# Performance work log

Hardware: AMD Instinct MI355X
Metric: run time of the kernel (lower is better)

Reference implementation:

```python
import jax, jax.numpy as jnp
import numpy as np

NUM_EXPERTS = 8
TOP_K = 2


def setup_inputs() -> dict:
    key = jax.random.key(0)
    k1, k2, k3, k4, k5 = jax.random.split(key, 5)
    H, F, E = 1024, 4096, NUM_EXPERTS
    s = 0.02
    return {
        "hidden_states": jax.random.normal(k1, (2, 2048, H), jnp.float32),
        "w_router": jax.random.normal(k2, (E, H), jnp.float32) * s,
        "w1": jax.random.normal(k3, (E, F, H), jnp.float32) * s,
        "w2": jax.random.normal(k4, (E, H, F), jnp.float32) * s,
        "w3": jax.random.normal(k5, (E, F, H), jnp.float32) * s,
    }


def reference(hidden_states, w_router, w1, w2, w3):
    B, S, H = hidden_states.shape
    x = hidden_states.reshape(-1, H)  # [T, H]
    T = x.shape[0]
    # router (nn.Linear, no bias): logits = x @ W^T
    router_logits = x @ w_router.T  # [T, E]
    probs = jax.nn.softmax(router_logits.astype(jnp.float32), axis=-1)
    top_w, top_e = jax.lax.top_k(probs, TOP_K)  # [T, K]
    top_w = top_w / jnp.sum(top_w, axis=-1, keepdims=True)
    top_w = top_w.astype(x.dtype)
    # dense per-token gate matrix [T, E]; zero where expert not selected
    gates = jnp.zeros((T, NUM_EXPERTS), x.dtype).at[
        jnp.arange(T)[:, None], top_e
    ].add(top_w)
    out = jnp.zeros_like(x)
    for e in range(NUM_EXPERTS):  # fixed small expert loop
        h = jax.nn.silu(x @ w1[e].T) * (x @ w3[e].T)  # [T, F]
        out = out + gates[:, e:e + 1] * (h @ w2[e].T)
    return out.reshape(B, S, H), router_logits
```

## Files before the change

kernel.cpp:

```cpp
#include <hip/hip_runtime.h>
#include <hip/hip_bf16.h>
#include <stdint.h>

#define T_TOK 4096
#define H_DIM 1024
#define F_DIM 4096
#define NE 8
#define MG_BLKS 40

typedef float    f32x4  __attribute__((ext_vector_type(4)));
typedef __bf16   bf16x8 __attribute__((ext_vector_type(8)));
typedef uint16_t u16x8  __attribute__((ext_vector_type(8)));

#define AS1 __attribute__((address_space(1)))
#define AS3 __attribute__((address_space(3)))

__device__ __forceinline__ uint16_t f2bf(float f) {
  return __builtin_bit_cast(uint16_t, __float2bfloat16(f));
}

__device__ __forceinline__ void gld16(const void* g, void* l) {
  __builtin_amdgcn_global_load_lds((const AS1 void*)g, (AS3 void*)l, 16, 0, 0);
}

__device__ __forceinline__ bf16x8 ldsB_frag(const float* tile, int row, int kg) {
  const int p0 = (2 * kg) ^ (row & 15);
  const int p1 = (2 * kg + 1) ^ (row & 15);
  const f32x4 v0 = *(const f32x4*)&tile[row * 64 + p0 * 4];
  const f32x4 v1 = *(const f32x4*)&tile[row * 64 + p1 * 4];
  u16x8 ub;
#pragma unroll
  for (int j = 0; j < 4; ++j) { ub[j] = f2bf(v0[j]); ub[j + 4] = f2bf(v1[j]); }
  return __builtin_bit_cast(bf16x8, ub);
}

__global__ __launch_bounds__(256) void router_k(
    const float* __restrict__ x, const float* __restrict__ wr,
    float* __restrict__ logits, uint16_t* __restrict__ xb,
    int* __restrict__ pairTok, float* __restrict__ pairGate,
    int* __restrict__ tokSlot, int* __restrict__ cnt)
{
  const int lane = threadIdx.x & 63;
  const int wid  = threadIdx.x >> 6;
  const int t    = blockIdx.x * 4 + wid;

  const float* xp = x + (size_t)t * H_DIM + lane * 16;
  f32x4 xv[4];
#pragma unroll
  for (int i = 0; i < 4; ++i) xv[i] = *(const f32x4*)(xp + 4 * i);

  u16x8 o0, o1;
#pragma unroll
  for (int j = 0; j < 4; ++j) {
    o0[j] = f2bf(xv[0][j]); o0[j + 4] = f2bf(xv[1][j]);
    o1[j] = f2bf(xv[2][j]); o1[j + 4] = f2bf(xv[3][j]);
  }
  uint16_t* xbp = xb + (size_t)t * H_DIM + lane * 16;
  *(u16x8*)xbp       = o0;
  *(u16x8*)(xbp + 8) = o1;

  float s[NE];
#pragma unroll
  for (int e = 0; e < NE; ++e) {
    const float* wp = wr + e * H_DIM + lane * 16;
    float acc = 0.f;
#pragma unroll
    for (int i = 0; i < 4; ++i) {
      f32x4 wv = *(const f32x4*)(wp + 4 * i);
#pragma unroll
      for (int j = 0; j < 4; ++j) acc += xv[i][j] * wv[j];
    }
#pragma unroll
    for (int off = 32; off > 0; off >>= 1) acc += __shfl_xor(acc, off, 64);
    s[e] = acc;
  }

  if (lane == 0) {
#pragma unroll
    for (int e = 0; e < NE; ++e) logits[t * NE + e] = s[e];
    int e1 = 0;
#pragma unroll
    for (int e = 1; e < NE; ++e) if (s[e] > s[e1]) e1 = e;
    int e2 = (e1 == 0) ? 1 : 0;
#pragma unroll
    for (int e = 0; e < NE; ++e)
      if (e != e1 && e != e2 && s[e] > s[e2]) e2 = e;
    const float d  = s[e2] - s[e1];
    const float g1 = 1.f / (1.f + __expf(d));
    const float g2 = 1.f - g1;
    int i1 = atomicAdd(cnt + e1, 1);
    pairTok[e1 * T_TOK + i1] = t;  pairGate[e1 * T_TOK + i1] = g1;
    int i2 = atomicAdd(cnt + e2, 1);
    pairTok[e2 * T_TOK + i2] = t;  pairGate[e2 * T_TOK + i2] = g2;
    int4 sl; sl.x = e1; sl.y = i1; sl.z = e2; sl.w = i2;
    ((int4*)tokSlot)[t] = sl;
  }
}

__global__ void prefix_k(const int* __restrict__ cnt, int* __restrict__ base) {
  if (threadIdx.x == 0) {
    int b = 0;
#pragma unroll
    for (int e = 0; e < NE; ++e) { base[e] = b; b += (cnt[e] + 255) & ~255; }
    base[NE] = b;
  }
}

__global__ __launch_bounds__(256, 2) void ffn1_k(
    const uint16_t* __restrict__ xb, const float* __restrict__ w1,
    const float* __restrict__ w3, uint16_t* __restrict__ hbuf,
    const int* __restrict__ pairTok, const float* __restrict__ pairGate,
    const int* __restrict__ cnt, const int* __restrict__ base)
{
  const int mg0 = blockIdx.y * 256;
  if (mg0 >= base[NE]) return;
  int e = 0;
#pragma unroll
  for (int k = 1; k < NE; ++k) if (mg0 >= base[k]) e = k;
  const int m0   = mg0 - base[e];
  const int cnte = cnt[e];
  const int n0   = blockIdx.x * 64;
  const int tid  = threadIdx.x;
  const int lane = tid & 63;
  const int wid  = tid >> 6;
  const int wm   = (wid >> 1) * 128;
  const int wn   = (wid & 1) * 32;

  __shared__ __align__(16) uint16_t lsA [256 * 64];
  __shared__ __align__(16) float    lsB1[ 64 * 64];
  __shared__ __align__(16) float    lsB3[ 64 * 64];

  const float* w1e = w1 + (size_t)e * F_DIM * H_DIM;
  const float* w3e = w3 + (size_t)e * F_DIM * H_DIM;

  const uint16_t* asrc[8];
#pragma unroll
  for (int q = 0; q < 8; ++q) {
    const int c = q * 256 + tid;
    const int row = c >> 3, pos = c & 7;
    const int kc  = pos ^ (row & 7);
    int ar = m0 + row; if (ar >= cnte) ar = cnte - 1;
    const int tok = pairTok[e * T_TOK + ar];
    asrc[q] = xb + (size_t)tok * H_DIM + kc * 8;
  }
  const float* b1src[4];
  const float* b3src[4];
#pragma unroll
  for (int q = 0; q < 4; ++q) {
    const int c = q * 256 + tid;
    const int row = c >> 4, pos = c & 15;
    const int kc  = pos ^ (row & 15);
    b1src[q] = w1e + (size_t)(n0 + row) * H_DIM + kc * 4;
    b3src[q] = w3e + (size_t)(n0 + row) * H_DIM + kc * 4;
  }

  const f32x4 fz = {0.f, 0.f, 0.f, 0.f};
  f32x4 acc1[8][2], acc3[8][2];
#pragma unroll
  for (int i = 0; i < 8; ++i)
#pragma unroll
    for (int j = 0; j < 2; ++j) { acc1[i][j] = fz; acc3[i][j] = fz; }

  for (int kt = 0; kt < H_DIM; kt += 64) {
    __syncthreads();
#pragma unroll
    for (int q = 0; q < 8; ++q)
      gld16(asrc[q] + kt, &lsA[(q * 256 + tid) * 8]);
#pragma unroll
    for (int q = 0; q < 4; ++q) {
      gld16(b1src[q] + kt, &lsB1[(q * 256 + tid) * 4]);
      gld16(b3src[q] + kt, &lsB3[(q * 256 + tid) * 4]);
    }
    __syncthreads();
#pragma unroll
    for (int ks = 0; ks < 2; ++ks) {
      const int kg = ks * 4 + (lane >> 4);
      bf16x8 af[8], b1f[2], b3f[2];
#pragma unroll
      for (int i = 0; i < 8; ++i) {
        const int ar = wm + i * 16 + (lane & 15);
        af[i] = *(const bf16x8*)&lsA[ar * 64 + ((kg ^ (ar & 7)) * 8)];
      }
#pragma unroll
      for (int j = 0; j < 2; ++j) {
        const int br = wn + j * 16 + (lane & 15);
        b1f[j] = ldsB_frag(lsB1, br, kg);
        b3f[j] = ldsB_frag(lsB3, br, kg);
      }
#pragma unroll
      for (int i = 0; i < 8; ++i)
#pragma unroll
        for (int j = 0; j < 2; ++j) {
          acc1[i][j] = __builtin_amdgcn_mfma_f32_16x16x32_bf16(af[i], b1f[j], acc1[i][j], 0, 0, 0);
          acc3[i][j] = __builtin_amdgcn_mfma_f32_16x16x32_bf16(af[i], b3f[j], acc3[i][j], 0, 0, 0);
        }
    }
  }

  const int be = base[e];
#pragma unroll
  for (int i = 0; i < 8; ++i) {
#pragma unroll
    for (int r = 0; r < 4; ++r) {
      const int lrow = m0 + wm + i * 16 + (lane >> 4) * 4 + r;
      if (lrow < cnte) {
        const float g = pairGate[e * T_TOK + lrow];
        uint16_t* hp = hbuf + (size_t)(be + lrow) * F_DIM + n0 + wn + (lane & 15);
#pragma unroll
        for (int j = 0; j < 2; ++j) {
          const float a  = acc1[i][j][r];
          const float hv = g * (a / (1.f + __expf(-a))) * acc3[i][j][r];
          hp[j * 16] = f2bf(hv);
        }
      }
    }
  }
}

__global__ __launch_bounds__(256, 2) void ffn2_k(
    const uint16_t* __restrict__ hbuf, const float* __restrict__ w2,
    uint16_t* __restrict__ y, const int* __restrict__ cnt,
    const int* __restrict__ base)
{
  const int mg0 = blockIdx.y * 256;
  if (mg0 >= base[NE]) return;
  int e = 0;
#pragma unroll
  for (int k = 1; k < NE; ++k) if (mg0 >= base[k]) e = k;
  const int m0   = mg0 - base[e];
  const int cnte = cnt[e];
  const int n0   = blockIdx.x * 128;
  const int tid  = threadIdx.x;
  const int lane = tid & 63;
  const int wid  = tid >> 6;
  const int wm   = (wid >> 1) * 128;
  const int wn   = (wid & 1) * 64;

  __shared__ __align__(16) uint16_t lsA[256 * 64];
  __shared__ __align__(16) float    lsB[128 * 64];

  const int be = base[e];
  const float* w2e = w2 + (size_t)e * H_DIM * F_DIM;

  const uint16_t* asrc[8];
#pragma unroll
  for (int q = 0; q < 8; ++q) {
    const int c = q * 256 + tid;
    const int row = c >> 3, pos = c & 7;
    const int kc  = pos ^ (row & 7);
    int rr = m0 + row; if (rr >= cnte) rr = cnte - 1;
    asrc[q] = hbuf + (size_t)(be + rr) * F_DIM + kc * 8;
  }
  const float* bsrc[8];
#pragma unroll
  for (int q = 0; q < 8; ++q) {
    const int c = q * 256 + tid;
    const int row = c >> 4, pos = c & 15;
    const int kc  = pos ^ (row & 15);
    bsrc[q] = w2e + (size_t)(n0 + row) * F_DIM + kc * 4;
  }

  const f32x4 fz = {0.f, 0.f, 0.f, 0.f};
  f32x4 acc[8][4];
#pragma unroll
  for (int i = 0; i < 8; ++i)
#pragma unroll
    for (int j = 0; j < 4; ++j) acc[i][j] = fz;

  for (int kt = 0; kt < F_DIM; kt += 64) {
    __syncthreads();
#pragma unroll
    for (int q = 0; q < 8; ++q)
      gld16(asrc[q] + kt, &lsA[(q * 256 + tid) * 8]);
#pragma unroll
    for (int q = 0; q < 8; ++q)
      gld16(bsrc[q] + kt, &lsB[(q * 256 + tid) * 4]);
    __syncthreads();
#pragma unroll
    for (int ks = 0; ks < 2; ++ks) {
      const int kg = ks * 4 + (lane >> 4);
      bf16x8 af[8], bf[4];
#pragma unroll
      for (int i = 0; i < 8; ++i) {
        const int ar = wm + i * 16 + (lane & 15);
        af[i] = *(const bf16x8*)&lsA[ar * 64 + ((kg ^ (ar & 7)) * 8)];
      }
#pragma unroll
      for (int j = 0; j < 4; ++j) {
        const int br = wn + j * 16 + (lane & 15);
        bf[j] = ldsB_frag(lsB, br, kg);
      }
#pragma unroll
      for (int i = 0; i < 8; ++i)
#pragma unroll
        for (int j = 0; j < 4; ++j)
          acc[i][j] = __builtin_amdgcn_mfma_f32_16x16x32_bf16(af[i], bf[j], acc[i][j], 0, 0, 0);
    }
  }

#pragma unroll
  for (int i = 0; i < 8; ++i) {
#pragma unroll
    for (int r = 0; r < 4; ++r) {
      const int lrow = m0 + wm + i * 16 + (lane >> 4) * 4 + r;
      if (lrow < cnte) {
        uint16_t* yp = y + (size_t)(be + lrow) * H_DIM + n0 + wn + (lane & 15);
#pragma unroll
        for (int j = 0; j < 4; ++j)
          yp[j * 16] = f2bf(acc[i][j][r]);
      }
    }
  }
}

__global__ __launch_bounds__(256) void combine_k(
    const uint16_t* __restrict__ y, const int* __restrict__ tokSlot,
    const int* __restrict__ base, float* __restrict__ out)
{
  const int t = blockIdx.x * 2 + (threadIdx.x >> 7);
  const int c = (threadIdx.x & 127) * 8;
  const int4 s = ((const int4*)tokSlot)[t];
  const uint16_t* y1 = y + (size_t)(base[s.x] + s.y) * H_DIM + c;
  const uint16_t* y2 = y + (size_t)(base[s.z] + s.w) * H_DIM + c;
  const u16x8 a = *(const u16x8*)y1;
  const u16x8 b = *(const u16x8*)y2;
  float* op = out + (size_t)t * H_DIM + c;
  f32x4 o0, o1;
#pragma unroll
  for (int j = 0; j < 4; ++j) {
    o0[j] = __bfloat162float(__hip_bfloat16_raw{a[j]}) +
            __bfloat162float(__hip_bfloat16_raw{b[j]});
    o1[j] = __bfloat162float(__hip_bfloat16_raw{a[j + 4]}) +
            __bfloat162float(__hip_bfloat16_raw{b[j + 4]});
  }
  *(f32x4*)op       = o0;
  *(f32x4*)(op + 4) = o1;
}

extern "C" void kernel_launch(void* const* d_in, const int* in_sizes, int n_in,
                              void* d_out, int out_size, void* d_ws, size_t ws_size,
                              hipStream_t stream)
{
  const float* x  = (const float*)d_in[0];
  const float* wr = (const float*)d_in[1];
  const float* w1 = (const float*)d_in[2];
  const float* w2 = (const float*)d_in[3];
  const float* w3 = (const float*)d_in[4];
  float* out    = (float*)d_out;
  float* logits = out + (size_t)T_TOK * H_DIM;

  uint8_t* ws = (uint8_t*)d_ws;
  const size_t PADROWS  = (size_t)MG_BLKS * 256;
  const size_t XB_OFF   = 0;
  const size_t HB_OFF   = XB_OFF + (size_t)T_TOK * H_DIM * 2;
  const size_t Y_OFF    = HB_OFF + PADROWS * F_DIM * 2;
  const size_t PT_OFF   = Y_OFF + PADROWS * H_DIM * 2;
  const size_t PG_OFF   = PT_OFF + (size_t)NE * T_TOK * 4;
  const size_t TS_OFF   = PG_OFF + (size_t)NE * T_TOK * 4;
  const size_t CNT_OFF  = TS_OFF + (size_t)T_TOK * 16;
  const size_t BASE_OFF = CNT_OFF + 64;
  const size_t NEED     = BASE_OFF + 64;
  if (ws_size < NEED) return;

  uint16_t* xb      = (uint16_t*)(ws + XB_OFF);
  uint16_t* hb      = (uint16_t*)(ws + HB_OFF);
  uint16_t* yb      = (uint16_t*)(ws + Y_OFF);
  int*      pairTok = (int*)(ws + PT_OFF);
  float*    pairGate= (float*)(ws + PG_OFF);
  int*      tokSlot = (int*)(ws + TS_OFF);
  int*      cnt     = (int*)(ws + CNT_OFF);
  int*      basep   = (int*)(ws + BASE_OFF);

  hipMemsetAsync(cnt, 0, 64, stream);
  router_k<<<T_TOK / 4, 256, 0, stream>>>(x, wr, logits, xb, pairTok, pairGate, tokSlot, cnt);
  prefix_k<<<1, 64, 0, stream>>>(cnt, basep);
  ffn1_k<<<dim3(F_DIM / 64, MG_BLKS, 1), 256, 0, stream>>>(xb, w1, w3, hb, pairTok, pairGate, cnt, basep);
  ffn2_k<<<dim3(H_DIM / 128, MG_BLKS, 1), 256, 0, stream>>>(hb, w2, yb, cnt, basep);
  combine_k<<<T_TOK / 2, 256, 0, stream>>>(yb, tokSlot, basep, out);
}
```

Before: 468.4 us.

## Fuse combine into ffn2 via atomic scatter, split-K ffn2, inline prefix

```diff
diff --git a/kernel.cpp b/kernel.cpp
--- a/kernel.cpp
+++ b/kernel.cpp
@@ -34,11 +34,18 @@
   return __builtin_bit_cast(bf16x8, ub);
 }
 
+__device__ __forceinline__ void calc_base(const int* cnt, int* base9) {
+  int b = 0;
+#pragma unroll
+  for (int e = 0; e < NE; ++e) { base9[e] = b; b += (cnt[e] + 255) & ~255; }
+  base9[NE] = b;
+}
+
 __global__ __launch_bounds__(256) void router_k(
     const float* __restrict__ x, const float* __restrict__ wr,
     float* __restrict__ logits, uint16_t* __restrict__ xb,
     int* __restrict__ pairTok, float* __restrict__ pairGate,
-    int* __restrict__ tokSlot, int* __restrict__ cnt)
+    int* __restrict__ cnt)
 {
   const int lane = threadIdx.x & 63;
   const int wid  = threadIdx.x >> 6;
@@ -92,17 +99,6 @@
     pairTok[e1 * T_TOK + i1] = t;  pairGate[e1 * T_TOK + i1] = g1;
     int i2 = atomicAdd(cnt + e2, 1);
     pairTok[e2 * T_TOK + i2] = t;  pairGate[e2 * T_TOK + i2] = g2;
-    int4 sl; sl.x = e1; sl.y = i1; sl.z = e2; sl.w = i2;
-    ((int4*)tokSlot)[t] = sl;
-  }
-}
-
-__global__ void prefix_k(const int* __restrict__ cnt, int* __restrict__ base) {
-  if (threadIdx.x == 0) {
-    int b = 0;
-#pragma unroll
-    for (int e = 0; e < NE; ++e) { base[e] = b; b += (cnt[e] + 255) & ~255; }
-    base[NE] = b;
   }
 }
 
@@ -110,8 +106,10 @@
     const uint16_t* __restrict__ xb, const float* __restrict__ w1,
     const float* __restrict__ w3, uint16_t* __restrict__ hbuf,
     const int* __restrict__ pairTok, const float* __restrict__ pairGate,
-    const int* __restrict__ cnt, const int* __restrict__ base)
+    const int* __restrict__ cnt)
 {
+  int base[NE + 1];
+  calc_base(cnt, base);
   const int mg0 = blockIdx.y * 256;
   if (mg0 >= base[NE]) return;
   int e = 0;
@@ -201,15 +199,15 @@
 #pragma unroll
   for (int i = 0; i < 8; ++i) {
 #pragma unroll
-    for (int r = 0; r < 4; ++r) {
-      const int lrow = m0 + wm + i * 16 + (lane >> 4) * 4 + r;
+    for (int rr = 0; rr < 4; ++rr) {
+      const int lrow = m0 + wm + i * 16 + (lane >> 4) * 4 + rr;
       if (lrow < cnte) {
         const float g = pairGate[e * T_TOK + lrow];
         uint16_t* hp = hbuf + (size_t)(be + lrow) * F_DIM + n0 + wn + (lane & 15);
 #pragma unroll
         for (int j = 0; j < 2; ++j) {
-          const float a  = acc1[i][j][r];
-          const float hv = g * (a / (1.f + __expf(-a))) * acc3[i][j][r];
+          const float a  = acc1[i][j][rr];
+          const float hv = g * (a / (1.f + __expf(-a))) * acc3[i][j][rr];
           hp[j * 16] = f2bf(hv);
         }
       }
@@ -219,9 +217,11 @@
 
 __global__ __launch_bounds__(256, 2) void ffn2_k(
     const uint16_t* __restrict__ hbuf, const float* __restrict__ w2,
-    uint16_t* __restrict__ y, const int* __restrict__ cnt,
-    const int* __restrict__ base)
+    float* __restrict__ out, const int* __restrict__ pairTok,
+    const int* __restrict__ cnt)
 {
+  int base[NE + 1];
+  calc_base(cnt, base);
   const int mg0 = blockIdx.y * 256;
   if (mg0 >= base[NE]) return;
   int e = 0;
@@ -230,6 +230,7 @@
   const int m0   = mg0 - base[e];
   const int cnte = cnt[e];
   const int n0   = blockIdx.x * 128;
+  const int k0   = blockIdx.z * (F_DIM / 2);
   const int tid  = threadIdx.x;
   const int lane = tid & 63;
   const int wid  = tid >> 6;
@@ -249,7 +250,7 @@
     const int row = c >> 3, pos = c & 7;
     const int kc  = pos ^ (row & 7);
     int rr = m0 + row; if (rr >= cnte) rr = cnte - 1;
-    asrc[q] = hbuf + (size_t)(be + rr) * F_DIM + kc * 8;
+    asrc[q] = hbuf + (size_t)(be + rr) * F_DIM + k0 + kc * 8;
   }
   const float* bsrc[8];
 #pragma unroll
@@ -257,7 +258,7 @@
     const int c = q * 256 + tid;
     const int row = c >> 4, pos = c & 15;
     const int kc  = pos ^ (row & 15);
-    bsrc[q] = w2e + (size_t)(n0 + row) * F_DIM + kc * 4;
+    bsrc[q] = w2e + (size_t)(n0 + row) * F_DIM + k0 + kc * 4;
   }
 
   const f32x4 fz = {0.f, 0.f, 0.f, 0.f};
@@ -267,7 +268,7 @@
 #pragma unroll
     for (int j = 0; j < 4; ++j) acc[i][j] = fz;
 
-  for (int kt = 0; kt < F_DIM; kt += 64) {
+  for (int kt = 0; kt < F_DIM / 2; kt += 64) {
     __syncthreads();
 #pragma unroll
     for (int q = 0; q < 8; ++q)
@@ -301,40 +302,17 @@
 #pragma unroll
   for (int i = 0; i < 8; ++i) {
 #pragma unroll
-    for (int r = 0; r < 4; ++r) {
-      const int lrow = m0 + wm + i * 16 + (lane >> 4) * 4 + r;
+    for (int rr = 0; rr < 4; ++rr) {
+      const int lrow = m0 + wm + i * 16 + (lane >> 4) * 4 + rr;
       if (lrow < cnte) {
-        uint16_t* yp = y + (size_t)(be + lrow) * H_DIM + n0 + wn + (lane & 15);
+        const int t = pairTok[e * T_TOK + lrow];
+        float* op = out + (size_t)t * H_DIM + n0 + wn + (lane & 15);
 #pragma unroll
         for (int j = 0; j < 4; ++j)
-          yp[j * 16] = f2bf(acc[i][j][r]);
-      }
-    }
-  }
-}
-
-__global__ __launch_bounds__(256) void combine_k(
-    const uint16_t* __restrict__ y, const int* __restrict__ tokSlot,
-    const int* __restrict__ base, float* __restrict__ out)
-{
-  const int t = blockIdx.x * 2 + (threadIdx.x >> 7);
-  const int c = (threadIdx.x & 127) * 8;
-  const int4 s = ((const int4*)tokSlot)[t];
-  const uint16_t* y1 = y + (size_t)(base[s.x] + s.y) * H_DIM + c;
-  const uint16_t* y2 = y + (size_t)(base[s.z] + s.w) * H_DIM + c;
-  const u16x8 a = *(const u16x8*)y1;
-  const u16x8 b = *(const u16x8*)y2;
-  float* op = out + (size_t)t * H_DIM + c;
-  f32x4 o0, o1;
-#pragma unroll
-  for (int j = 0; j < 4; ++j) {
-    o0[j] = __bfloat162float(__hip_bfloat16_raw{a[j]}) +
-            __bfloat162float(__hip_bfloat16_raw{b[j]});
-    o1[j] = __bfloat162float(__hip_bfloat16_raw{a[j + 4]}) +
-            __bfloat162float(__hip_bfloat16_raw{b[j + 4]});
-  }
-  *(f32x4*)op       = o0;
-  *(f32x4*)(op + 4) = o1;
+          unsafeAtomicAdd(op + j * 16, acc[i][j][rr]);
+      }
+    }
+  }
 }
 
 extern "C" void kernel_launch(void* const* d_in, const int* in_sizes, int n_in,
@@ -353,28 +331,21 @@
   const size_t PADROWS  = (size_t)MG_BLKS * 256;
   const size_t XB_OFF   = 0;
   const size_t HB_OFF   = XB_OFF + (size_t)T_TOK * H_DIM * 2;
-  const size_t Y_OFF    = HB_OFF + PADROWS * F_DIM * 2;
-  const size_t PT_OFF   = Y_OFF + PADROWS * H_DIM * 2;
+  const size_t PT_OFF   = HB_OFF + PADROWS * F_DIM * 2;
   const size_t PG_OFF   = PT_OFF + (size_t)NE * T_TOK * 4;
-  const size_t TS_OFF   = PG_OFF + (size_t)NE * T_TOK * 4;
-  const size_t CNT_OFF  = TS_OFF + (size_t)T_TOK * 16;
-  const size_t BASE_OFF = CNT_OFF + 64;
-  const size_t NEED     = BASE_OFF + 64;
+  const size_t CNT_OFF  = PG_OFF + (size_t)NE * T_TOK * 4;
+  const size_t NEED     = CNT_OFF + 64;
   if (ws_size < NEED) return;
 
   uint16_t* xb      = (uint16_t*)(ws + XB_OFF);
   uint16_t* hb      = (uint16_t*)(ws + HB_OFF);
-  uint16_t* yb      = (uint16_t*)(ws + Y_OFF);
   int*      pairTok = (int*)(ws + PT_OFF);
   float*    pairGate= (float*)(ws + PG_OFF);
-  int*      tokSlot = (int*)(ws + TS_OFF);
   int*      cnt     = (int*)(ws + CNT_OFF);
-  int*      basep   = (int*)(ws + BASE_OFF);
-
+
+  hipMemsetAsync(out, 0, (size_t)T_TOK * H_DIM * sizeof(float), stream);
   hipMemsetAsync(cnt, 0, 64, stream);
-  router_k<<<T_TOK / 4, 256, 0, stream>>>(x, wr, logits, xb, pairTok, pairGate, tokSlot, cnt);
-  prefix_k<<<1, 64, 0, stream>>>(cnt, basep);
-  ffn1_k<<<dim3(F_DIM / 64, MG_BLKS, 1), 256, 0, stream>>>(xb, w1, w3, hb, pairTok, pairGate, cnt, basep);
-  ffn2_k<<<dim3(H_DIM / 128, MG_BLKS, 1), 256, 0, stream>>>(hb, w2, yb, cnt, basep);
-  combine_k<<<T_TOK / 2, 256, 0, stream>>>(yb, tokSlot, basep, out);
-}
+  router_k<<<T_TOK / 4, 256, 0, stream>>>(x, wr, logits, xb, pairTok, pairGate, cnt);
+  ffn1_k<<<dim3(F_DIM / 64, MG_BLKS, 1), 256, 0, stream>>>(xb, w1, w3, hb, pairTok, pairGate, cnt);
+  ffn2_k<<<dim3(H_DIM / 128, MG_BLKS, 2), 256, 0, stream>>>(hb, w2, out, pairTok, cnt);
+}
```

Result: slower. 507.7 us (+8.4%).

## Double-buffer ffn2 LDS tiles and fold prefix kernel into consumers

Applied to the files above, without the earlier changes.

```diff
diff --git a/kernel.cpp b/kernel.cpp
--- a/kernel.cpp
+++ b/kernel.cpp
@@ -32,6 +32,13 @@
 #pragma unroll
   for (int j = 0; j < 4; ++j) { ub[j] = f2bf(v0[j]); ub[j + 4] = f2bf(v1[j]); }
   return __builtin_bit_cast(bf16x8, ub);
+}
+
+__device__ __forceinline__ void calc_base(const int* cnt, int* base9) {
+  int b = 0;
+#pragma unroll
+  for (int e = 0; e < NE; ++e) { base9[e] = b; b += (cnt[e] + 255) & ~255; }
+  base9[NE] = b;
 }
 
 __global__ __launch_bounds__(256) void router_k(
@@ -97,21 +104,14 @@
   }
 }
 
-__global__ void prefix_k(const int* __restrict__ cnt, int* __restrict__ base) {
-  if (threadIdx.x == 0) {
-    int b = 0;
-#pragma unroll
-    for (int e = 0; e < NE; ++e) { base[e] = b; b += (cnt[e] + 255) & ~255; }
-    base[NE] = b;
-  }
-}
-
 __global__ __launch_bounds__(256, 2) void ffn1_k(
     const uint16_t* __restrict__ xb, const float* __restrict__ w1,
     const float* __restrict__ w3, uint16_t* __restrict__ hbuf,
     const int* __restrict__ pairTok, const float* __restrict__ pairGate,
-    const int* __restrict__ cnt, const int* __restrict__ base)
-{
+    const int* __restrict__ cnt)
+{
+  int base[NE + 1];
+  calc_base(cnt, base);
   const int mg0 = blockIdx.y * 256;
   if (mg0 >= base[NE]) return;
   int e = 0;
@@ -201,15 +201,15 @@
 #pragma unroll
   for (int i = 0; i < 8; ++i) {
 #pragma unroll
-    for (int r = 0; r < 4; ++r) {
-      const int lrow = m0 + wm + i * 16 + (lane >> 4) * 4 + r;
+    for (int rr = 0; rr < 4; ++rr) {
+      const int lrow = m0 + wm + i * 16 + (lane >> 4) * 4 + rr;
       if (lrow < cnte) {
         const float g = pairGate[e * T_TOK + lrow];
         uint16_t* hp = hbuf + (size_t)(be + lrow) * F_DIM + n0 + wn + (lane & 15);
 #pragma unroll
         for (int j = 0; j < 2; ++j) {
-          const float a  = acc1[i][j][r];
-          const float hv = g * (a / (1.f + __expf(-a))) * acc3[i][j][r];
+          const float a  = acc1[i][j][rr];
+          const float hv = g * (a / (1.f + __expf(-a))) * acc3[i][j][rr];
           hp[j * 16] = f2bf(hv);
         }
       }
@@ -217,11 +217,12 @@
   }
 }
 
-__global__ __launch_bounds__(256, 2) void ffn2_k(
+__global__ __launch_bounds__(256, 1) void ffn2_k(
     const uint16_t* __restrict__ hbuf, const float* __restrict__ w2,
-    uint16_t* __restrict__ y, const int* __restrict__ cnt,
-    const int* __restrict__ base)
-{
+    uint16_t* __restrict__ y, const int* __restrict__ cnt)
+{
+  int base[NE + 1];
+  calc_base(cnt, base);
   const int mg0 = blockIdx.y * 256;
   if (mg0 >= base[NE]) return;
   int e = 0;
@@ -236,8 +237,8 @@
   const int wm   = (wid >> 1) * 128;
   const int wn   = (wid & 1) * 64;
 
-  __shared__ __align__(16) uint16_t lsA[256 * 64];
-  __shared__ __align__(16) float    lsB[128 * 64];
+  __shared__ __align__(16) uint16_t lsA[2][256 * 64];
+  __shared__ __align__(16) float    lsB[2][128 * 64];
 
   const int be = base[e];
   const float* w2e = w2 + (size_t)e * H_DIM * F_DIM;
@@ -260,6 +261,33 @@
     bsrc[q] = w2e + (size_t)(n0 + row) * F_DIM + kc * 4;
   }
 
+#define STAGE2(buf, koff)                                                 \
+  {                                                                       \
+    _Pragma("unroll") for (int q = 0; q < 8; ++q)                         \
+      gld16(asrc[q] + (koff), &lsA[buf][(q * 256 + tid) * 8]);            \
+    _Pragma("unroll") for (int q = 0; q < 8; ++q)                         \
+      gld16(bsrc[q] + (koff), &lsB[buf][(q * 256 + tid) * 4]);            \
+  }
+
+#define COMPUTE2(cur)                                                     \
+  {                                                                       \
+    _Pragma("unroll") for (int ks = 0; ks < 2; ++ks) {                    \
+      const int kg = ks * 4 + (lane >> 4);                                \
+      bf16x8 af[8], bf[4];                                                \
+      _Pragma("unroll") for (int i = 0; i < 8; ++i) {                     \
+        const int ar = wm + i * 16 + (lane & 15);                         \
+        af[i] = *(const bf16x8*)&lsA[cur][ar * 64 + ((kg ^ (ar & 7)) * 8)]; \
+      }                                                                   \
+      _Pragma("unroll") for (int j = 0; j < 4; ++j) {                     \
+        const int br = wn + j * 16 + (lane & 15);                         \
+        bf[j] = ldsB_frag(lsB[cur], br, kg);                              \
+      }                                                                   \
+      _Pragma("unroll") for (int i = 0; i < 8; ++i)                       \
+        _Pragma("unroll") for (int j = 0; j < 4; ++j)                     \
+          acc[i][j] = __builtin_amdgcn_mfma_f32_16x16x32_bf16(af[i], bf[j], acc[i][j], 0, 0, 0); \
+    }                                                                     \
+  }
+
   const f32x4 fz = {0.f, 0.f, 0.f, 0.f};
   f32x4 acc[8][4];
 #pragma unroll
@@ -267,47 +295,38 @@
 #pragma unroll
     for (int j = 0; j < 4; ++j) acc[i][j] = fz;
 
-  for (int kt = 0; kt < F_DIM; kt += 64) {
-    __syncthreads();
-#pragma unroll
-    for (int q = 0; q < 8; ++q)
-      gld16(asrc[q] + kt, &lsA[(q * 256 + tid) * 8]);
-#pragma unroll
-    for (int q = 0; q < 8; ++q)
-      gld16(bsrc[q] + kt, &lsB[(q * 256 + tid) * 4]);
-    __syncthreads();
-#pragma unroll
-    for (int ks = 0; ks < 2; ++ks) {
-      const int kg = ks * 4 + (lane >> 4);
-      bf16x8 af[8], bf[4];
-#pragma unroll
-      for (int i = 0; i < 8; ++i) {
-        const int ar = wm + i * 16 + (lane & 15);
-        af[i] = *(const bf16x8*)&lsA[ar * 64 + ((kg ^ (ar & 7)) * 8)];
-      }
-#pragma unroll
-      for (int j = 0; j < 4; ++j) {
-        const int br = wn + j * 16 + (lane & 15);
-        bf[j] = ldsB_frag(lsB, br, kg);
-      }
-#pragma unroll
-      for (int i = 0; i < 8; ++i)
-#pragma unroll
-        for (int j = 0; j < 4; ++j)
-          acc[i][j] = __builtin_amdgcn_mfma_f32_16x16x32_bf16(af[i], bf[j], acc[i][j], 0, 0, 0);
-    }
-  }
+  const int NT = F_DIM / 64;
+  STAGE2(0, 0)
+  STAGE2(1, 64)
+
+  for (int t = 0; t < NT - 1; ++t) {
+    const int cur = t & 1;
+    asm volatile("s_waitcnt vmcnt(16)" ::: "memory");
+    __builtin_amdgcn_s_barrier();
+    __builtin_amdgcn_s_setprio(1);
+    COMPUTE2(cur)
+    __builtin_amdgcn_s_setprio(0);
+    __builtin_amdgcn_s_barrier();
+    if (t + 2 < NT) STAGE2(cur, (t + 2) * 64)
+  }
+  {
+    asm volatile("s_waitcnt vmcnt(0)" ::: "memory");
+    __builtin_amdgcn_s_barrier();
+    COMPUTE2((NT - 1) & 1)
+  }
+#undef STAGE2
+#undef COMPUTE2
 
 #pragma unroll
   for (int i = 0; i < 8; ++i) {
 #pragma unroll
-    for (int r = 0; r < 4; ++r) {
-      const int lrow = m0 + wm + i * 16 + (lane >> 4) * 4 + r;
+    for (int rr = 0; rr < 4; ++rr) {
+      const int lrow = m0 + wm + i * 16 + (lane >> 4) * 4 + rr;
       if (lrow < cnte) {
         uint16_t* yp = y + (size_t)(be + lrow) * H_DIM + n0 + wn + (lane & 15);
 #pragma unroll
         for (int j = 0; j < 4; ++j)
-          yp[j * 16] = f2bf(acc[i][j][r]);
+          yp[j * 16] = f2bf(acc[i][j][rr]);
       }
     }
   }
@@ -315,8 +334,10 @@
 
 __global__ __launch_bounds__(256) void combine_k(
     const uint16_t* __restrict__ y, const int* __restrict__ tokSlot,
-    const int* __restrict__ base, float* __restrict__ out)
-{
+    const int* __restrict__ cnt, float* __restrict__ out)
+{
+  int base[NE + 1];
+  calc_base(cnt, base);
   const int t = blockIdx.x * 2 + (threadIdx.x >> 7);
   const int c = (threadIdx.x & 127) * 8;
   const int4 s = ((const int4*)tokSlot)[t];
@@ -358,8 +379,7 @@
   const size_t PG_OFF   = PT_OFF + (size_t)NE * T_TOK * 4;
   const size_t TS_OFF   = PG_OFF + (size_t)NE * T_TOK * 4;
   const size_t CNT_OFF  = TS_OFF + (size_t)T_TOK * 16;
-  const size_t BASE_OFF = CNT_OFF + 64;
-  const size_t NEED     = BASE_OFF + 64;
+  const size_t NEED     = CNT_OFF + 64;
   if (ws_size < NEED) return;
 
   uint16_t* xb      = (uint16_t*)(ws + XB_OFF);
@@ -369,12 +389,10 @@
   float*    pairGate= (float*)(ws + PG_OFF);
   int*      tokSlot = (int*)(ws + TS_OFF);
   int*      cnt     = (int*)(ws + CNT_OFF);
-  int*      basep   = (int*)(ws + BASE_OFF);
 
   hipMemsetAsync(cnt, 0, 64, stream);
   router_k<<<T_TOK / 4, 256, 0, stream>>>(x, wr, logits, xb, pairTok, pairGate, tokSlot, cnt);
-  prefix_k<<<1, 64, 0, stream>>>(cnt, basep);
-  ffn1_k<<<dim3(F_DIM / 64, MG_BLKS, 1), 256, 0, stream>>>(xb, w1, w3, hb, pairTok, pairGate, cnt, basep);
-  ffn2_k<<<dim3(H_DIM / 128, MG_BLKS, 1), 256, 0, stream>>>(hb, w2, yb, cnt, basep);
-  combine_k<<<T_TOK / 2, 256, 0, stream>>>(yb, tokSlot, basep, out);
-}
+  ffn1_k<<<dim3(F_DIM / 64, MG_BLKS, 1), 256, 0, stream>>>(xb, w1, w3, hb, pairTok, pairGate, cnt);
+  ffn2_k<<<dim3(H_DIM / 128, MG_BLKS, 1), 256, 0, stream>>>(hb, w2, yb, cnt);
+  combine_k<<<T_TOK / 2, 256, 0, stream>>>(yb, tokSlot, cnt, out);
+}
```

Result: slower. 570.9 us (+21.9%).
